# Performance work log

Hardware: AMD Instinct MI355X
Metric: run time of the kernel (lower is better)

## Reference

```python
import jax, jax.numpy as jnp
import numpy as np

B, S, H, NH = 8, 1024, 1024, 16
DH = H // NH


def setup_inputs() -> dict:
    key = jax.random.key(0)
    ks = jax.random.split(key, 16)
    inp = {
        'v': jax.random.normal(ks[0], (B, S, H), jnp.float32),
        'k': jax.random.normal(ks[1], (B, S, H), jnp.float32),
        'q': jax.random.normal(ks[2], (B, S, H), jnp.float32),
        'r': jax.random.normal(ks[3], (B, S, H), jnp.float32),
        'mask': jax.random.randint(ks[4], (B, 1, 1, S), 0, 2).astype(jnp.bool_),
    }
    scale = 1.0 / np.sqrt(H)
    names = ['Wv', 'Wk', 'Wq', 'Wr', 'Wm']
    for i, n in enumerate(names):
        inp[n] = jax.random.normal(ks[5 + i], (H, H), jnp.float32) * scale
        inp['b' + n[1:]] = jnp.zeros((H,), jnp.float32)
    return inp


def _heads(x, W, b):
    # torch Linear: x @ W.T + b, then split heads -> [B, NH, S, DH]
    y = jnp.einsum('bsh,oh->bso', x, W) + b
    return y.reshape(B, S, NH, DH).transpose(0, 2, 1, 3)


def reference(v, k, q, r, mask, Wv, bv, Wk, bk, Wq, bq, Wr, br, Wm, bm):
    vh = _heads(v, Wv, bv)
    kh = _heads(k, Wk, bk)
    qh = _heads(q, Wq, bq)
    rh = _heads(r, Wr, br)
    # relation-augmented scores: (QK^T + RK^T) / sqrt(d_k)
    scores = jnp.einsum('bhqd,bhkd->bhqk', qh + rh, kh) / jnp.sqrt(jnp.asarray(DH, qh.dtype))
    scores = jnp.where(mask, jnp.asarray(-1e9, scores.dtype), scores)
    att = jax.nn.softmax(scores, axis=-1)  # dropout = identity in eval
    out = jnp.einsum('bhqk,bhkd->bhqd', att, vh)
    out = out.transpose(0, 2, 1, 3).reshape(B, S, H)
    return jnp.einsum('bsh,oh->bso', out, Wm) + bm
```

## Files before the change

kernel.cpp:

```cpp
#include <hip/hip_runtime.h>
#include <hip/hip_bf16.h>
#include <stdint.h>

typedef __attribute__((ext_vector_type(4))) float f32x4;
typedef __attribute__((ext_vector_type(8))) short s16x8;
typedef __attribute__((ext_vector_type(4))) short s16x4;
typedef __attribute__((ext_vector_type(4))) int i32x4;

typedef const __attribute__((address_space(1))) unsigned glb_u32;
typedef __attribute__((address_space(3))) unsigned lds_u32;

#define DEVI __device__ __forceinline__

DEVI short f2b(float f) {
    union { float f; unsigned u; } v; v.f = f;
    unsigned r = v.u + 0x7fffu + ((v.u >> 16) & 1u);
    return (short)(r >> 16);
}

DEVI float vexp2(float x) {
    float r;
    asm("v_exp_f32 %0, %1" : "=v"(r) : "v"(x));
    return r;
}

DEVI unsigned cvtpk(float lo, float hi) {
    unsigned d;
    asm("v_cvt_pk_bf16_f32 %0, %1, %2" : "=v"(d) : "v"(lo), "v"(hi));
    return d;
}

DEVI s16x8 pack8(const f32x4& a, const f32x4& b) {
    union { unsigned u[4]; s16x8 v; } w;
    w.u[0] = cvtpk(a[0], a[1]);
    w.u[1] = cvtpk(a[2], a[3]);
    w.u[2] = cvtpk(b[0], b[1]);
    w.u[3] = cvtpk(b[2], b[3]);
    return w.v;
}

#define QSCL 0.18033688011112042f
#define MASKV -1.4426950408889634e9f

struct Ptr7 { const float* p[7]; };

__global__ __launch_bounds__(256) void cvt_all(Ptr7 t, short* __restrict__ vb,
                                               short* __restrict__ kb,
                                               short* __restrict__ Wb) {
    int bid = blockIdx.x;
    const float* s; short* d; int off;
    if (bid < 4096)      { s = t.p[0]; d = vb; off = bid; }
    else if (bid < 8192) { s = t.p[1]; d = kb; off = bid - 4096; }
    else {
        int w = (bid - 8192) >> 9;
        s = t.p[2 + w]; d = Wb + (size_t)w * 1048576u; off = (bid - 8192) & 511;
    }
    int i = (off * 256 + threadIdx.x) * 8;
    f32x4 a = *(const f32x4*)(s + i);
    f32x4 b = *(const f32x4*)(s + i + 4);
    *(s16x8*)(d + i) = pack8(a, b);
}

template<int AF32, int OUTMODE, int TWO>
DEVI void gemm_body(int logical,
                    const void* A0_, const void* A1_,
                    const short* W0, const short* W1,
                    const float* b0, const float* b1,
                    void* C_, short* As, short* Ws)
{
    constexpr int K = 1024, N = 1024;
    const int tid = threadIdx.x;
    const int lane = tid & 63, wid = tid >> 6;
    const int wm = wid >> 1, wn = wid & 1;
    const int r = lane & 15, g = lane >> 4;
    const int n0 = (logical & 7) * 128, m0 = (logical >> 3) * 128;

    auto stage_async = [&](int buf, int kt) {
        int kk = kt * 32;
        const short* Ap = (const short*)A0_; const short* Wp = W0;
        if (TWO && kk >= 1024) { Ap = (const short*)A1_; Wp = W1; kk &= 1023; }
#pragma unroll
        for (int i = 0; i < 2; ++i) {
            int row = wid * 32 + i * 16 + (lane >> 2);
            const short* ga = Ap + (size_t)(m0 + row) * K + kk + (lane & 3) * 8;
            const short* gw = Wp + (size_t)(n0 + row) * K + kk + (lane & 3) * 8;
            __builtin_amdgcn_global_load_lds((glb_u32*)ga,
                (lds_u32*)(As + buf * 4096 + (wid * 32 + i * 16) * 32), 16, 0, 0);
            __builtin_amdgcn_global_load_lds((glb_u32*)gw,
                (lds_u32*)(Ws + buf * 4096 + (wid * 32 + i * 16) * 32), 16, 0, 0);
        }
    };

    const int srow = tid >> 1, shalf = tid & 1;
    f32x4 a0g, a1g, a2g, a3g;
    s16x8 wg0, wg1;
    auto load_regs = [&](int kt) {
        int kk = kt * 32;
        const float* Ap = (const float*)A0_; const short* Wp = W0;
        if (TWO && kk >= 1024) { Ap = (const float*)A1_; Wp = W1; kk &= 1023; }
        const short* wp = Wp + (size_t)(n0 + srow) * K + kk + shalf * 16;
        wg0 = *(const s16x8*)wp;
        wg1 = *(const s16x8*)(wp + 8);
        const float* ap = Ap + (size_t)(m0 + srow) * K + kk + shalf * 16;
        a0g = *(const f32x4*)ap;       a1g = *(const f32x4*)(ap + 4);
        a2g = *(const f32x4*)(ap + 8); a3g = *(const f32x4*)(ap + 12);
    };
    auto store_lds = [&](int buf) {
        s16x8 s0 = pack8(a0g, a1g);
        s16x8 s1 = pack8(a2g, a3g);
        char* ab = (char*)(As + buf * 4096);
        *(s16x8*)(ab + srow * 64 + shalf * 32) = s0;
        *(s16x8*)(ab + srow * 64 + shalf * 32 + 16) = s1;
        char* wb = (char*)(Ws + buf * 4096);
        *(s16x8*)(wb + srow * 64 + shalf * 32) = wg0;
        *(s16x8*)(wb + srow * 64 + shalf * 32 + 16) = wg1;
    };

    f32x4 z = {0.f, 0.f, 0.f, 0.f};
    f32x4 acc[4][4];
#pragma unroll
    for (int i = 0; i < 4; ++i)
#pragma unroll
        for (int j = 0; j < 4; ++j) acc[i][j] = z;

    auto compute = [&](int buf) {
        s16x8 af[4], bfr[4];
#pragma unroll
        for (int f = 0; f < 4; ++f) {
            af[f]  = *(const s16x8*)(As + buf * 4096 + (wm * 64 + f * 16 + r) * 32 + g * 8);
            bfr[f] = *(const s16x8*)(Ws + buf * 4096 + (wn * 64 + f * 16 + r) * 32 + g * 8);
        }
#pragma unroll
        for (int i = 0; i < 4; ++i)
#pragma unroll
            for (int j = 0; j < 4; ++j)
                acc[i][j] = __builtin_amdgcn_mfma_f32_16x16x32_bf16(af[i], bfr[j], acc[i][j], 0, 0, 0);
    };

    constexpr int NK = TWO ? 64 : 32;
    if constexpr (AF32) { load_regs(0); store_lds(0); }
    else stage_async(0, 0);
    __syncthreads();
    int buf = 0;
    for (int kt = 0; kt < NK; ++kt) {
        if (kt + 1 < NK) {
            if constexpr (AF32) load_regs(kt + 1);
            else stage_async(buf ^ 1, kt + 1);
        }
        compute(buf);
        if (AF32 && kt + 1 < NK) store_lds(buf ^ 1);
        __syncthreads();
        buf ^= 1;
    }

#pragma unroll
    for (int j = 0; j < 4; ++j) {
        int col = n0 + wn * 64 + j * 16 + r;
        float bb = b0[col];
        if (TWO) bb += b1[col];
#pragma unroll
        for (int i = 0; i < 4; ++i) {
            int rowb = m0 + wm * 64 + i * 16 + g * 4;
            if constexpr (OUTMODE == 2) {
                int bb_ = rowb >> 10, tok = rowb & 1023;
                int tokp = (tok & ~31) | (((tok >> 2) & 3) << 3) | (((tok >> 4) & 1) << 2);
                short* dst = (short*)C_ + ((size_t)(bb_ * 16 + (col >> 6))) * 65536
                           + (size_t)(col & 63) * 1024 + tokp;
                s16x4 o;
#pragma unroll
                for (int q = 0; q < 4; ++q) o[q] = f2b(acc[i][j][q] + bb);
                *(s16x4*)dst = o;
            } else {
#pragma unroll
                for (int q = 0; q < 4; ++q) {
                    float val = acc[i][j][q] + bb;
                    if constexpr (OUTMODE == 1)
                        ((float*)C_)[(size_t)(rowb + q) * N + col] = val;
                    else if constexpr (OUTMODE == 3)
                        ((short*)C_)[(size_t)(rowb + q) * N + col] = f2b(val * QSCL);
                    else
                        ((short*)C_)[(size_t)(rowb + q) * N + col] = f2b(val);
                }
            }
        }
    }
}

__global__ __launch_bounds__(256) void proj_all(
    const short* __restrict__ vb, const short* __restrict__ kb,
    const float* __restrict__ qf, const float* __restrict__ rf,
    const short* __restrict__ Wb,
    const float* __restrict__ bv, const float* __restrict__ bk,
    const float* __restrict__ bq, const float* __restrict__ br,
    short* __restrict__ vtb, short* __restrict__ khb, short* __restrict__ qrb)
{
    __shared__ alignas(16) short As[2 * 128 * 32];
    __shared__ alignas(16) short Ws[2 * 128 * 32];
    const int bid = blockIdx.x;
    const int sub = bid >> 9, lbid = bid & 511;
    const int logical = (lbid & 7) * 64 + (lbid >> 3);
    if (sub == 0)
        gemm_body<0, 2, 0>(logical, vb, nullptr, Wb, nullptr, bv, nullptr, vtb, As, Ws);
    else if (sub == 1)
        gemm_body<0, 0, 0>(logical, kb, nullptr, Wb + 1048576u, nullptr, bk, nullptr, khb, As, Ws);
    else
        gemm_body<1, 3, 1>(logical, qf, rf, Wb + 2097152u, Wb + 3145728u, bq, br, qrb, As, Ws);
}

template<int AF32, int OUTMODE, int TWO>
__global__ __launch_bounds__(256) void gemm_nt(
    const void* __restrict__ A0_, const void* __restrict__ A1_,
    const short* __restrict__ W0, const short* __restrict__ W1,
    const float* __restrict__ b0, const float* __restrict__ b1,
    void* __restrict__ C_)
{
    __shared__ alignas(16) short As[2 * 128 * 32];
    __shared__ alignas(16) short Ws[2 * 128 * 32];
    const int bid = blockIdx.x;
    const int logical = (bid & 7) * 64 + (bid >> 3);
    gemm_body<AF32, OUTMODE, TWO>(logical, A0_, A1_, W0, W1, b0, b1, C_, As, Ws);
}

__global__ __launch_bounds__(256) void attn_fwd(
    const short* __restrict__ qrh, const short* __restrict__ kh,
    const short* __restrict__ vT, const int* __restrict__ mask,
    short* __restrict__ outp)
{
    const int bh = blockIdx.x;
    const int b = bh >> 4, h = bh & 15;
    const int qt = blockIdx.y;
    const int tid = threadIdx.x, lane = tid & 63, wid = tid >> 6;
    const int r = lane & 15, g = lane >> 4;

    __shared__ alignas(16) short Ks[64 * 64];
    __shared__ alignas(16) short Vs[64 * 64];
    __shared__ alignas(16) float mb[1024];

    {
        i32x4 mi = *(const i32x4*)(mask + b * 1024 + tid * 4);
        f32x4 mv;
#pragma unroll
        for (int j = 0; j < 4; ++j) mv[j] = mi[j] ? MASKV : 0.f;
        *(f32x4*)&mb[tid * 4] = mv;
    }

    const int q0 = qt * 128 + wid * 32;
    const short* qbA = qrh + (size_t)(b * 1024 + q0 + r) * 1024 + h * 64;
    const short* qbB = qbA + 16 * 1024;
    s16x8 qA0 = *(const s16x8*)(qbA + g * 8);
    s16x8 qA1 = *(const s16x8*)(qbA + 32 + g * 8);
    s16x8 qB0 = *(const s16x8*)(qbB + g * 8);
    s16x8 qB1 = *(const s16x8*)(qbB + 32 + g * 8);

    f32x4 z = {0.f, 0.f, 0.f, 0.f};
    f32x4 oA[4], oB[4];
#pragma unroll
    for (int i = 0; i < 4; ++i) { oA[i] = z; oB[i] = z; }
    float lA = 0.f, lB = 0.f;

    const int srow = tid >> 2, sq = tid & 3;
    const short* kg = kh + (size_t)(b * 1024 + srow) * 1024 + h * 64 + sq * 16;
    const short* vg = vT + ((size_t)(b * 16 + h)) * 65536 + (size_t)srow * 1024 + sq * 16;
    const int p0s = (sq * 2) ^ (srow & 7), p1s = (sq * 2 + 1) ^ (srow & 7);

    s16x8 kr0, kr1, vr0, vr1;
    auto stage_load = [&](int t) {
        const short* kp = kg + (size_t)(t * 64) * 1024;
        kr0 = *(const s16x8*)kp; kr1 = *(const s16x8*)(kp + 8);
        const short* vp = vg + t * 64;
        vr0 = *(const s16x8*)vp; vr1 = *(const s16x8*)(vp + 8);
    };
    auto stage_write = [&]() {
        char* kb2 = (char*)Ks;
        *(s16x8*)(kb2 + srow * 128 + p0s * 16) = kr0;
        *(s16x8*)(kb2 + srow * 128 + p1s * 16) = kr1;
        char* vb2 = (char*)Vs;
        *(s16x8*)(vb2 + srow * 128 + p0s * 16) = vr0;
        *(s16x8*)(vb2 + srow * 128 + p1s * 16) = vr1;
    };

    stage_load(0);
    for (int t = 0; t < 16; ++t) {
        if (t) __syncthreads();
        stage_write();
        __syncthreads();
        if (t < 15) stage_load(t + 1);

        f32x4 pA[4], pB[4];
        char* kb2 = (char*)Ks;
        float tsA = 0.f, tsB = 0.f;
#pragma unroll
        for (int fn = 0; fn < 4; ++fn) {
            int row = fn * 16 + r;
            s16x8 kfa = *(const s16x8*)(kb2 + row * 128 + ((g ^ (row & 7)) << 4));
            s16x8 kfb = *(const s16x8*)(kb2 + row * 128 + (((4 + g) ^ (row & 7)) << 4));
            f32x4 cA = __builtin_amdgcn_mfma_f32_16x16x32_bf16(kfa, qA0, z, 0, 0, 0);
            cA = __builtin_amdgcn_mfma_f32_16x16x32_bf16(kfb, qA1, cA, 0, 0, 0);
            f32x4 cB = __builtin_amdgcn_mfma_f32_16x16x32_bf16(kfa, qB0, z, 0, 0, 0);
            cB = __builtin_amdgcn_mfma_f32_16x16x32_bf16(kfb, qB1, cB, 0, 0, 0);
            f32x4 mv = *(const f32x4*)&mb[t * 64 + fn * 16 + g * 4];
#pragma unroll
            for (int qi = 0; qi < 4; ++qi) {
                float eA = vexp2(cA[qi] + mv[qi]); pA[fn][qi] = eA; tsA += eA;
                float eB = vexp2(cB[qi] + mv[qi]); pB[fn][qi] = eB; tsB += eB;
            }
        }
        tsA += __shfl_xor(tsA, 16); tsA += __shfl_xor(tsA, 32);
        tsB += __shfl_xor(tsB, 16); tsB += __shfl_xor(tsB, 32);
        lA += tsA; lB += tsB;

        char* vb2 = (char*)Vs;
#pragma unroll
        for (int ks = 0; ks < 2; ++ks) {
            s16x8 pbA = pack8(pA[2 * ks], pA[2 * ks + 1]);
            s16x8 pbB = pack8(pB[2 * ks], pB[2 * ks + 1]);
#pragma unroll
            for (int df = 0; df < 4; ++df) {
                int row = df * 16 + r;
                int slot = (ks * 4 + g) ^ (row & 7);
                s16x8 vf = *(const s16x8*)(vb2 + row * 128 + (slot << 4));
                oA[df] = __builtin_amdgcn_mfma_f32_16x16x32_bf16(vf, pbA, oA[df], 0, 0, 0);
                oB[df] = __builtin_amdgcn_mfma_f32_16x16x32_bf16(vf, pbB, oB[df], 0, 0, 0);
            }
        }
    }

    float ivA = 1.f / lA, ivB = 1.f / lB;
#pragma unroll
    for (int df = 0; df < 4; ++df) {
        s16x4 oa, ob;
#pragma unroll
        for (int qi = 0; qi < 4; ++qi) {
            oa[qi] = f2b(oA[df][qi] * ivA);
            ob[qi] = f2b(oB[df][qi] * ivB);
        }
        *(s16x4*)&outp[(size_t)(b * 1024 + q0 + r) * 1024 + h * 64 + df * 16 + g * 4] = oa;
        *(s16x4*)&outp[(size_t)(b * 1024 + q0 + 16 + r) * 1024 + h * 64 + df * 16 + g * 4] = ob;
    }
}

extern "C" void kernel_launch(void* const* d_in, const int* in_sizes, int n_in,
                              void* d_out, int out_size, void* d_ws, size_t ws_size,
                              hipStream_t stream) {
    const float* v  = (const float*)d_in[0];
    const float* k  = (const float*)d_in[1];
    const float* q  = (const float*)d_in[2];
    const float* rr = (const float*)d_in[3];
    const int* mask = (const int*)d_in[4];
    const float* Wv = (const float*)d_in[5];  const float* bv = (const float*)d_in[6];
    const float* Wk = (const float*)d_in[7];  const float* bk = (const float*)d_in[8];
    const float* Wq = (const float*)d_in[9];  const float* bq = (const float*)d_in[10];
    const float* Wr = (const float*)d_in[11]; const float* br = (const float*)d_in[12];
    const float* Wm = (const float*)d_in[13]; const float* bm = (const float*)d_in[14];

    const size_t MB = 1048576u;
    const size_t NEED = 90u * MB;
    if (ws_size < NEED) return;

    char* ws = (char*)d_ws;
    short* Wb  = (short*)ws;
    short* vb  = (short*)(ws + 10u * MB);
    short* kb  = (short*)(ws + 26u * MB);
    short* vtb = (short*)(ws + 42u * MB);
    short* khb = (short*)(ws + 58u * MB);
    short* qrb = (short*)(ws + 74u * MB);
    short* att = vb;

    Ptr7 t7;
    t7.p[0] = v;  t7.p[1] = k;
    t7.p[2] = Wv; t7.p[3] = Wk; t7.p[4] = Wq; t7.p[5] = Wr; t7.p[6] = Wm;
    cvt_all<<<dim3(10752), 256, 0, stream>>>(t7, vb, kb, Wb);

    proj_all<<<dim3(1536), 256, 0, stream>>>(vb, kb, q, rr, Wb,
                                             bv, bk, bq, br, vtb, khb, qrb);

    attn_fwd<<<dim3(128, 8), 256, 0, stream>>>(qrb, khb, vtb, mask, att);

    gemm_nt<0, 1, 0><<<dim3(512), 256, 0, stream>>>(att, nullptr, Wb + 4194304u,
                                                    nullptr, bm, nullptr, (float*)d_out);
}
```

Baseline: 223.3 us.

## Use 256-row M tiles for V and K projections in fused projection kernel

The V and K projection GEMMs inside proj_all now use 256x128 output tiles, with each wave computing 128x64 (8x4 MFMA fragments). This halves their block count, so the combined launch drops from 1536 to 1024 blocks while the Q+R GEMM keeps 128x128 tiles. The aim is more reuse of each weight tile per load and less global traffic. In exchange the kernel uses more LDS and accumulator registers, which lowers occupancy for every block, including the Q+R path that shares the kernel.

```diff
diff --git a/kernel.cpp b/kernel.cpp
--- a/kernel.cpp
+++ b/kernel.cpp
@@ -61,7 +61,7 @@
     *(s16x8*)(d + i) = pack8(a, b);
 }
 
-template<int AF32, int OUTMODE, int TWO>
+template<int AF32, int OUTMODE, int TWO, int FAT>
 DEVI void gemm_body(int logical,
                     const void* A0_, const void* A1_,
                     const short* W0, const short* W1,
@@ -69,25 +69,33 @@
                     void* C_, short* As, short* Ws)
 {
     constexpr int K = 1024, N = 1024;
+    constexpr int BM   = FAT ? 256 : 128;
+    constexpr int MI   = FAT ? 8 : 4;
+    constexpr int WMS  = FAT ? 128 : 64;
+    constexpr int ABUF = BM * 32;
     const int tid = threadIdx.x;
     const int lane = tid & 63, wid = tid >> 6;
     const int wm = wid >> 1, wn = wid & 1;
     const int r = lane & 15, g = lane >> 4;
-    const int n0 = (logical & 7) * 128, m0 = (logical >> 3) * 128;
+    const int n0 = (logical & 7) * 128, m0 = (logical >> 3) * BM;
 
     auto stage_async = [&](int buf, int kt) {
         int kk = kt * 32;
         const short* Ap = (const short*)A0_; const short* Wp = W0;
         if (TWO && kk >= 1024) { Ap = (const short*)A1_; Wp = W1; kk &= 1023; }
 #pragma unroll
+        for (int i = 0; i < (FAT ? 4 : 2); ++i) {
+            int rbase = wid * (FAT ? 64 : 32) + i * 16;
+            const short* ga = Ap + (size_t)(m0 + rbase + (lane >> 2)) * K + kk + (lane & 3) * 8;
+            __builtin_amdgcn_global_load_lds((glb_u32*)ga,
+                (lds_u32*)(As + buf * ABUF + rbase * 32), 16, 0, 0);
+        }
+#pragma unroll
         for (int i = 0; i < 2; ++i) {
-            int row = wid * 32 + i * 16 + (lane >> 2);
-            const short* ga = Ap + (size_t)(m0 + row) * K + kk + (lane & 3) * 8;
-            const short* gw = Wp + (size_t)(n0 + row) * K + kk + (lane & 3) * 8;
-            __builtin_amdgcn_global_load_lds((glb_u32*)ga,
-                (lds_u32*)(As + buf * 4096 + (wid * 32 + i * 16) * 32), 16, 0, 0);
+            int rbase = wid * 32 + i * 16;
+            const short* gw = Wp + (size_t)(n0 + rbase + (lane >> 2)) * K + kk + (lane & 3) * 8;
             __builtin_amdgcn_global_load_lds((glb_u32*)gw,
-                (lds_u32*)(Ws + buf * 4096 + (wid * 32 + i * 16) * 32), 16, 0, 0);
+                (lds_u32*)(Ws + buf * 4096 + rbase * 32), 16, 0, 0);
         }
     };
 
@@ -108,7 +116,7 @@
     auto store_lds = [&](int buf) {
         s16x8 s0 = pack8(a0g, a1g);
         s16x8 s1 = pack8(a2g, a3g);
-        char* ab = (char*)(As + buf * 4096);
+        char* ab = (char*)(As + buf * ABUF);
         *(s16x8*)(ab + srow * 64 + shalf * 32) = s0;
         *(s16x8*)(ab + srow * 64 + shalf * 32 + 16) = s1;
         char* wb = (char*)(Ws + buf * 4096);
@@ -117,21 +125,22 @@
     };
 
     f32x4 z = {0.f, 0.f, 0.f, 0.f};
-    f32x4 acc[4][4];
-#pragma unroll
-    for (int i = 0; i < 4; ++i)
+    f32x4 acc[MI][4];
+#pragma unroll
+    for (int i = 0; i < MI; ++i)
 #pragma unroll
         for (int j = 0; j < 4; ++j) acc[i][j] = z;
 
     auto compute = [&](int buf) {
-        s16x8 af[4], bfr[4];
-#pragma unroll
-        for (int f = 0; f < 4; ++f) {
-            af[f]  = *(const s16x8*)(As + buf * 4096 + (wm * 64 + f * 16 + r) * 32 + g * 8);
+        s16x8 af[MI], bfr[4];
+#pragma unroll
+        for (int f = 0; f < MI; ++f)
+            af[f] = *(const s16x8*)(As + buf * ABUF + (wm * WMS + f * 16 + r) * 32 + g * 8);
+#pragma unroll
+        for (int f = 0; f < 4; ++f)
             bfr[f] = *(const s16x8*)(Ws + buf * 4096 + (wn * 64 + f * 16 + r) * 32 + g * 8);
-        }
-#pragma unroll
-        for (int i = 0; i < 4; ++i)
+#pragma unroll
+        for (int i = 0; i < MI; ++i)
 #pragma unroll
             for (int j = 0; j < 4; ++j)
                 acc[i][j] = __builtin_amdgcn_mfma_f32_16x16x32_bf16(af[i], bfr[j], acc[i][j], 0, 0, 0);
@@ -159,8 +168,8 @@
         float bb = b0[col];
         if (TWO) bb += b1[col];
 #pragma unroll
-        for (int i = 0; i < 4; ++i) {
-            int rowb = m0 + wm * 64 + i * 16 + g * 4;
+        for (int i = 0; i < MI; ++i) {
+            int rowb = m0 + wm * WMS + i * 16 + g * 4;
             if constexpr (OUTMODE == 2) {
                 int bb_ = rowb >> 10, tok = rowb & 1023;
                 int tokp = (tok & ~31) | (((tok >> 2) & 3) << 3) | (((tok >> 4) & 1) << 2);
@@ -194,17 +203,22 @@
     const float* __restrict__ bq, const float* __restrict__ br,
     short* __restrict__ vtb, short* __restrict__ khb, short* __restrict__ qrb)
 {
-    __shared__ alignas(16) short As[2 * 128 * 32];
+    __shared__ alignas(16) short As[2 * 256 * 32];
     __shared__ alignas(16) short Ws[2 * 128 * 32];
     const int bid = blockIdx.x;
-    const int sub = bid >> 9, lbid = bid & 511;
-    const int logical = (lbid & 7) * 64 + (lbid >> 3);
-    if (sub == 0)
-        gemm_body<0, 2, 0>(logical, vb, nullptr, Wb, nullptr, bv, nullptr, vtb, As, Ws);
-    else if (sub == 1)
-        gemm_body<0, 0, 0>(logical, kb, nullptr, Wb + 1048576u, nullptr, bk, nullptr, khb, As, Ws);
-    else
-        gemm_body<1, 3, 1>(logical, qf, rf, Wb + 2097152u, Wb + 3145728u, bq, br, qrb, As, Ws);
+    if (bid < 256) {
+        int lb = bid;
+        int logical = (lb & 7) * 32 + (lb >> 3);
+        gemm_body<0, 2, 0, 1>(logical, vb, nullptr, Wb, nullptr, bv, nullptr, vtb, As, Ws);
+    } else if (bid < 512) {
+        int lb = bid - 256;
+        int logical = (lb & 7) * 32 + (lb >> 3);
+        gemm_body<0, 0, 0, 1>(logical, kb, nullptr, Wb + 1048576u, nullptr, bk, nullptr, khb, As, Ws);
+    } else {
+        int lb = bid - 512;
+        int logical = (lb & 7) * 64 + (lb >> 3);
+        gemm_body<1, 3, 1, 0>(logical, qf, rf, Wb + 2097152u, Wb + 3145728u, bq, br, qrb, As, Ws);
+    }
 }
 
 template<int AF32, int OUTMODE, int TWO>
@@ -218,7 +232,7 @@
     __shared__ alignas(16) short Ws[2 * 128 * 32];
     const int bid = blockIdx.x;
     const int logical = (bid & 7) * 64 + (bid >> 3);
-    gemm_body<AF32, OUTMODE, TWO>(logical, A0_, A1_, W0, W1, b0, b1, C_, As, Ws);
+    gemm_body<AF32, OUTMODE, TWO, 0>(logical, A0_, A1_, W0, W1, b0, b1, C_, As, Ws);
 }
 
 __global__ __launch_bounds__(256) void attn_fwd(
@@ -371,7 +385,7 @@
     t7.p[2] = Wv; t7.p[3] = Wk; t7.p[4] = Wq; t7.p[5] = Wr; t7.p[6] = Wm;
     cvt_all<<<dim3(10752), 256, 0, stream>>>(t7, vb, kb, Wb);
 
-    proj_all<<<dim3(1536), 256, 0, stream>>>(vb, kb, q, rr, Wb,
+    proj_all<<<dim3(1024), 256, 0, stream>>>(vb, kb, q, rr, Wb,
                                              bv, bk, bq, br, vtb, khb, qrb);
 
     attn_fwd<<<dim3(128, 8), 256, 0, stream>>>(qrb, khb, vtb, mask, att);
```

Measured after the change: 232.9 us. 4.3% more time.

## Replace LDS-staged GEMM with direct-from-global register-prefetch GEMM and pre-convert q/r

Applied to the files above, without the earlier changes.

The GEMM body no longer stages tiles through shared memory. Each wave loads its MFMA fragments straight from global memory into registers, double-buffered across k-steps, so the __syncthreads barriers go away. The fp32 q and r inputs are now converted to bf16 in the conversion kernel, and the projection is split into separate q/r and v/k launches, with outputs aliased into the freed buffers. The trade-off is that each wave re-reads operands from global memory with no LDS reuse across waves in a block, which leans on L2 and raises global traffic. The extra conversion pass also adds bytes written and read.

```diff
diff --git a/kernel.cpp b/kernel.cpp
--- a/kernel.cpp
+++ b/kernel.cpp
@@ -6,9 +6,6 @@
 typedef __attribute__((ext_vector_type(8))) short s16x8;
 typedef __attribute__((ext_vector_type(4))) short s16x4;
 typedef __attribute__((ext_vector_type(4))) int i32x4;
-
-typedef const __attribute__((address_space(1))) unsigned glb_u32;
-typedef __attribute__((address_space(3))) unsigned lds_u32;
 
 #define DEVI __device__ __forceinline__
 
@@ -42,18 +39,22 @@
 #define QSCL 0.18033688011112042f
 #define MASKV -1.4426950408889634e9f
 
-struct Ptr7 { const float* p[7]; };
-
-__global__ __launch_bounds__(256) void cvt_all(Ptr7 t, short* __restrict__ vb,
+struct Ptr9 { const float* p[9]; };
+
+__global__ __launch_bounds__(256) void cvt_all(Ptr9 t, short* __restrict__ vb,
                                                short* __restrict__ kb,
+                                               short* __restrict__ qb,
+                                               short* __restrict__ rb,
                                                short* __restrict__ Wb) {
     int bid = blockIdx.x;
     const float* s; short* d; int off;
-    if (bid < 4096)      { s = t.p[0]; d = vb; off = bid; }
-    else if (bid < 8192) { s = t.p[1]; d = kb; off = bid - 4096; }
+    if (bid < 4096)       { s = t.p[0]; d = vb; off = bid; }
+    else if (bid < 8192)  { s = t.p[1]; d = kb; off = bid - 4096; }
+    else if (bid < 12288) { s = t.p[2]; d = qb; off = bid - 8192; }
+    else if (bid < 16384) { s = t.p[3]; d = rb; off = bid - 12288; }
     else {
-        int w = (bid - 8192) >> 9;
-        s = t.p[2 + w]; d = Wb + (size_t)w * 1048576u; off = (bid - 8192) & 511;
+        int w = (bid - 16384) >> 9;
+        s = t.p[4 + w]; d = Wb + (size_t)w * 1048576u; off = (bid - 16384) & 511;
     }
     int i = (off * 256 + threadIdx.x) * 8;
     f32x4 a = *(const f32x4*)(s + i);
@@ -61,12 +62,11 @@
     *(s16x8*)(d + i) = pack8(a, b);
 }
 
-template<int AF32, int OUTMODE, int TWO>
-DEVI void gemm_body(int logical,
-                    const void* A0_, const void* A1_,
-                    const short* W0, const short* W1,
-                    const float* b0, const float* b1,
-                    void* C_, short* As, short* Ws)
+template<int OUTMODE, int TWO>
+DEVI void dgemm_body(int logical,
+                     const short* A0, const short* A1,
+                     const short* W0, const short* W1,
+                     const float* b0, const float* b1, void* C_)
 {
     constexpr int K = 1024, N = 1024;
     const int tid = threadIdx.x;
@@ -75,47 +75,6 @@
     const int r = lane & 15, g = lane >> 4;
     const int n0 = (logical & 7) * 128, m0 = (logical >> 3) * 128;
 
-    auto stage_async = [&](int buf, int kt) {
-        int kk = kt * 32;
-        const short* Ap = (const short*)A0_; const short* Wp = W0;
-        if (TWO && kk >= 1024) { Ap = (const short*)A1_; Wp = W1; kk &= 1023; }
-#pragma unroll
-        for (int i = 0; i < 2; ++i) {
-            int row = wid * 32 + i * 16 + (lane >> 2);
-            const short* ga = Ap + (size_t)(m0 + row) * K + kk + (lane & 3) * 8;
-            const short* gw = Wp + (size_t)(n0 + row) * K + kk + (lane & 3) * 8;
-            __builtin_amdgcn_global_load_lds((glb_u32*)ga,
-                (lds_u32*)(As + buf * 4096 + (wid * 32 + i * 16) * 32), 16, 0, 0);
-            __builtin_amdgcn_global_load_lds((glb_u32*)gw,
-                (lds_u32*)(Ws + buf * 4096 + (wid * 32 + i * 16) * 32), 16, 0, 0);
-        }
-    };
-
-    const int srow = tid >> 1, shalf = tid & 1;
-    f32x4 a0g, a1g, a2g, a3g;
-    s16x8 wg0, wg1;
-    auto load_regs = [&](int kt) {
-        int kk = kt * 32;
-        const float* Ap = (const float*)A0_; const short* Wp = W0;
-        if (TWO && kk >= 1024) { Ap = (const float*)A1_; Wp = W1; kk &= 1023; }
-        const short* wp = Wp + (size_t)(n0 + srow) * K + kk + shalf * 16;
-        wg0 = *(const s16x8*)wp;
-        wg1 = *(const s16x8*)(wp + 8);
-        const float* ap = Ap + (size_t)(m0 + srow) * K + kk + shalf * 16;
-        a0g = *(const f32x4*)ap;       a1g = *(const f32x4*)(ap + 4);
-        a2g = *(const f32x4*)(ap + 8); a3g = *(const f32x4*)(ap + 12);
-    };
-    auto store_lds = [&](int buf) {
-        s16x8 s0 = pack8(a0g, a1g);
-        s16x8 s1 = pack8(a2g, a3g);
-        char* ab = (char*)(As + buf * 4096);
-        *(s16x8*)(ab + srow * 64 + shalf * 32) = s0;
-        *(s16x8*)(ab + srow * 64 + shalf * 32 + 16) = s1;
-        char* wb = (char*)(Ws + buf * 4096);
-        *(s16x8*)(wb + srow * 64 + shalf * 32) = wg0;
-        *(s16x8*)(wb + srow * 64 + shalf * 32 + 16) = wg1;
-    };
-
     f32x4 z = {0.f, 0.f, 0.f, 0.f};
     f32x4 acc[4][4];
 #pragma unroll
@@ -123,35 +82,48 @@
 #pragma unroll
         for (int j = 0; j < 4; ++j) acc[i][j] = z;
 
-    auto compute = [&](int buf) {
-        s16x8 af[4], bfr[4];
+    auto half = [&](const short* Ap, const short* Wp) {
+        const short* ab[4];
+        const short* wb[4];
 #pragma unroll
         for (int f = 0; f < 4; ++f) {
-            af[f]  = *(const s16x8*)(As + buf * 4096 + (wm * 64 + f * 16 + r) * 32 + g * 8);
-            bfr[f] = *(const s16x8*)(Ws + buf * 4096 + (wn * 64 + f * 16 + r) * 32 + g * 8);
-        }
-#pragma unroll
-        for (int i = 0; i < 4; ++i)
-#pragma unroll
-            for (int j = 0; j < 4; ++j)
-                acc[i][j] = __builtin_amdgcn_mfma_f32_16x16x32_bf16(af[i], bfr[j], acc[i][j], 0, 0, 0);
+            ab[f] = Ap + (size_t)(m0 + wm * 64 + f * 16 + r) * K + g * 8;
+            wb[f] = Wp + (size_t)(n0 + wn * 64 + f * 16 + r) * K + g * 8;
+        }
+        s16x8 aX[4], wX[4], aY[4], wY[4];
+#pragma unroll
+        for (int f = 0; f < 4; ++f) {
+            aX[f] = *(const s16x8*)ab[f];
+            wX[f] = *(const s16x8*)wb[f];
+        }
+#pragma unroll
+        for (int kt = 0; kt < 32; kt += 2) {
+#pragma unroll
+            for (int f = 0; f < 4; ++f) {
+                aY[f] = *(const s16x8*)(ab[f] + (kt + 1) * 32);
+                wY[f] = *(const s16x8*)(wb[f] + (kt + 1) * 32);
+            }
+#pragma unroll
+            for (int i = 0; i < 4; ++i)
+#pragma unroll
+                for (int j = 0; j < 4; ++j)
+                    acc[i][j] = __builtin_amdgcn_mfma_f32_16x16x32_bf16(aX[i], wX[j], acc[i][j], 0, 0, 0);
+            if (kt + 2 < 32) {
+#pragma unroll
+                for (int f = 0; f < 4; ++f) {
+                    aX[f] = *(const s16x8*)(ab[f] + (kt + 2) * 32);
+                    wX[f] = *(const s16x8*)(wb[f] + (kt + 2) * 32);
+                }
+            }
+#pragma unroll
+            for (int i = 0; i < 4; ++i)
+#pragma unroll
+                for (int j = 0; j < 4; ++j)
+                    acc[i][j] = __builtin_amdgcn_mfma_f32_16x16x32_bf16(aY[i], wY[j], acc[i][j], 0, 0, 0);
+        }
     };
-
-    constexpr int NK = TWO ? 64 : 32;
-    if constexpr (AF32) { load_regs(0); store_lds(0); }
-    else stage_async(0, 0);
-    __syncthreads();
-    int buf = 0;
-    for (int kt = 0; kt < NK; ++kt) {
-        if (kt + 1 < NK) {
-            if constexpr (AF32) load_regs(kt + 1);
-            else stage_async(buf ^ 1, kt + 1);
-        }
-        compute(buf);
-        if (AF32 && kt + 1 < NK) store_lds(buf ^ 1);
-        __syncthreads();
-        buf ^= 1;
-    }
+    half(A0, W0);
+    if constexpr (TWO) half(A1, W1);
 
 #pragma unroll
     for (int j = 0; j < 4; ++j) {
@@ -186,39 +158,39 @@
     }
 }
 
-__global__ __launch_bounds__(256) void proj_all(
+__global__ __launch_bounds__(256) void proj_qr(
+    const short* __restrict__ qb, const short* __restrict__ rb,
+    const short* __restrict__ Wq, const short* __restrict__ Wr,
+    const float* __restrict__ bq, const float* __restrict__ br,
+    short* __restrict__ qrb)
+{
+    const int bid = blockIdx.x;
+    const int logical = (bid & 7) * 64 + (bid >> 3);
+    dgemm_body<3, 1>(logical, qb, rb, Wq, Wr, bq, br, qrb);
+}
+
+__global__ __launch_bounds__(256) void proj_vk(
     const short* __restrict__ vb, const short* __restrict__ kb,
-    const float* __restrict__ qf, const float* __restrict__ rf,
     const short* __restrict__ Wb,
     const float* __restrict__ bv, const float* __restrict__ bk,
-    const float* __restrict__ bq, const float* __restrict__ br,
-    short* __restrict__ vtb, short* __restrict__ khb, short* __restrict__ qrb)
-{
-    __shared__ alignas(16) short As[2 * 128 * 32];
-    __shared__ alignas(16) short Ws[2 * 128 * 32];
+    short* __restrict__ vtb, short* __restrict__ khb)
+{
     const int bid = blockIdx.x;
-    const int sub = bid >> 9, lbid = bid & 511;
-    const int logical = (lbid & 7) * 64 + (lbid >> 3);
-    if (sub == 0)
-        gemm_body<0, 2, 0>(logical, vb, nullptr, Wb, nullptr, bv, nullptr, vtb, As, Ws);
-    else if (sub == 1)
-        gemm_body<0, 0, 0>(logical, kb, nullptr, Wb + 1048576u, nullptr, bk, nullptr, khb, As, Ws);
+    const int lb = bid & 511;
+    const int logical = (lb & 7) * 64 + (lb >> 3);
+    if (bid < 512)
+        dgemm_body<2, 0>(logical, vb, nullptr, Wb, nullptr, bv, nullptr, vtb);
     else
-        gemm_body<1, 3, 1>(logical, qf, rf, Wb + 2097152u, Wb + 3145728u, bq, br, qrb, As, Ws);
-}
-
-template<int AF32, int OUTMODE, int TWO>
-__global__ __launch_bounds__(256) void gemm_nt(
-    const void* __restrict__ A0_, const void* __restrict__ A1_,
-    const short* __restrict__ W0, const short* __restrict__ W1,
-    const float* __restrict__ b0, const float* __restrict__ b1,
-    void* __restrict__ C_)
-{
-    __shared__ alignas(16) short As[2 * 128 * 32];
-    __shared__ alignas(16) short Ws[2 * 128 * 32];
+        dgemm_body<0, 0>(logical, kb, nullptr, Wb + 1048576u, nullptr, bk, nullptr, khb);
+}
+
+__global__ __launch_bounds__(256) void gemm_out(
+    const short* __restrict__ att, const short* __restrict__ Wm,
+    const float* __restrict__ bm, float* __restrict__ out)
+{
     const int bid = blockIdx.x;
     const int logical = (bid & 7) * 64 + (bid >> 3);
-    gemm_body<AF32, OUTMODE, TWO>(logical, A0_, A1_, W0, W1, b0, b1, C_, As, Ws);
+    dgemm_body<1, 0>(logical, att, nullptr, Wm, nullptr, bm, nullptr, out);
 }
 
 __global__ __launch_bounds__(256) void attn_fwd(
@@ -361,21 +333,23 @@
     short* Wb  = (short*)ws;
     short* vb  = (short*)(ws + 10u * MB);
     short* kb  = (short*)(ws + 26u * MB);
-    short* vtb = (short*)(ws + 42u * MB);
-    short* khb = (short*)(ws + 58u * MB);
+    short* qb  = (short*)(ws + 42u * MB);
+    short* rb  = (short*)(ws + 58u * MB);
     short* qrb = (short*)(ws + 74u * MB);
+    short* vtb = qb;
+    short* khb = rb;
     short* att = vb;
 
-    Ptr7 t7;
-    t7.p[0] = v;  t7.p[1] = k;
-    t7.p[2] = Wv; t7.p[3] = Wk; t7.p[4] = Wq; t7.p[5] = Wr; t7.p[6] = Wm;
-    cvt_all<<<dim3(10752), 256, 0, stream>>>(t7, vb, kb, Wb);
-
-    proj_all<<<dim3(1536), 256, 0, stream>>>(vb, kb, q, rr, Wb,
-                                             bv, bk, bq, br, vtb, khb, qrb);
+    Ptr9 t9;
+    t9.p[0] = v;  t9.p[1] = k;  t9.p[2] = q;  t9.p[3] = rr;
+    t9.p[4] = Wv; t9.p[5] = Wk; t9.p[6] = Wq; t9.p[7] = Wr; t9.p[8] = Wm;
+    cvt_all<<<dim3(18944), 256, 0, stream>>>(t9, vb, kb, qb, rb, Wb);
+
+    proj_qr<<<dim3(512), 256, 0, stream>>>(qb, rb, Wb + 2097152u, Wb + 3145728u,
+                                           bq, br, qrb);
+    proj_vk<<<dim3(1024), 256, 0, stream>>>(vb, kb, Wb, bv, bk, vtb, khb);
 
     attn_fwd<<<dim3(128, 8), 256, 0, stream>>>(qrb, khb, vtb, mask, att);
 
-    gemm_nt<0, 1, 0><<<dim3(512), 256, 0, stream>>>(att, nullptr, Wb + 4194304u,
-                                                    nullptr, bm, nullptr, (float*)d_out);
-}
+    gemm_out<<<dim3(512), 256, 0, stream>>>(att, Wb + 4194304u, bm, (float*)d_out);
+}
```

After: 380.8 us. 70.6% more time.

## Swizzle GEMM LDS layout and triple-buffer async loads with vmcnt waits

Applied to the files above, without the earlier changes.

Applies an XOR swizzle to the 16-byte chunks in the A/W LDS tiles, on the async global_load_lds path, the register store path and the MFMA fragment reads, to cut LDS bank conflicts. The bf16-input GEMM path moves from double buffering with a full __syncthreads per step to a three-stage ring: it prefetches two tiles ahead, waits with s_waitcnt vmcnt(4) and uses a bare s_barrier. This raises LDS use per block (48KB), which may reduce occupancy. The output GEMM becomes a non-template wrapper kernel.

```diff
diff --git a/kernel.cpp b/kernel.cpp
--- a/kernel.cpp
+++ b/kernel.cpp
@@ -75,19 +75,21 @@
     const int r = lane & 15, g = lane >> 4;
     const int n0 = (logical & 7) * 128, m0 = (logical >> 3) * 128;
 
-    auto stage_async = [&](int buf, int kt) {
+    const int arow = lane >> 2;
+    const int lq8 = ((lane & 3) ^ ((lane >> 3) & 3)) * 8;
+    auto stage = [&](int buf, int kt) {
         int kk = kt * 32;
         const short* Ap = (const short*)A0_; const short* Wp = W0;
         if (TWO && kk >= 1024) { Ap = (const short*)A1_; Wp = W1; kk &= 1023; }
 #pragma unroll
         for (int i = 0; i < 2; ++i) {
-            int row = wid * 32 + i * 16 + (lane >> 2);
-            const short* ga = Ap + (size_t)(m0 + row) * K + kk + (lane & 3) * 8;
-            const short* gw = Wp + (size_t)(n0 + row) * K + kk + (lane & 3) * 8;
+            int rbase = wid * 32 + i * 16;
+            const short* ga = Ap + (size_t)(m0 + rbase + arow) * K + kk + lq8;
+            const short* gw = Wp + (size_t)(n0 + rbase + arow) * K + kk + lq8;
             __builtin_amdgcn_global_load_lds((glb_u32*)ga,
-                (lds_u32*)(As + buf * 4096 + (wid * 32 + i * 16) * 32), 16, 0, 0);
+                (lds_u32*)(As + buf * 4096 + rbase * 32), 16, 0, 0);
             __builtin_amdgcn_global_load_lds((glb_u32*)gw,
-                (lds_u32*)(Ws + buf * 4096 + (wid * 32 + i * 16) * 32), 16, 0, 0);
+                (lds_u32*)(Ws + buf * 4096 + rbase * 32), 16, 0, 0);
         }
     };
 
@@ -108,12 +110,14 @@
     auto store_lds = [&](int buf) {
         s16x8 s0 = pack8(a0g, a1g);
         s16x8 s1 = pack8(a2g, a3g);
+        int sw = (srow >> 1) & 3;
+        int ph0 = (shalf * 2) ^ sw, ph1 = (shalf * 2 + 1) ^ sw;
         char* ab = (char*)(As + buf * 4096);
-        *(s16x8*)(ab + srow * 64 + shalf * 32) = s0;
-        *(s16x8*)(ab + srow * 64 + shalf * 32 + 16) = s1;
+        *(s16x8*)(ab + srow * 64 + ph0 * 16) = s0;
+        *(s16x8*)(ab + srow * 64 + ph1 * 16) = s1;
         char* wb = (char*)(Ws + buf * 4096);
-        *(s16x8*)(wb + srow * 64 + shalf * 32) = wg0;
-        *(s16x8*)(wb + srow * 64 + shalf * 32 + 16) = wg1;
+        *(s16x8*)(wb + srow * 64 + ph0 * 16) = wg0;
+        *(s16x8*)(wb + srow * 64 + ph1 * 16) = wg1;
     };
 
     f32x4 z = {0.f, 0.f, 0.f, 0.f};
@@ -123,12 +127,13 @@
 #pragma unroll
         for (int j = 0; j < 4; ++j) acc[i][j] = z;
 
+    const int sl = (g ^ ((r >> 1) & 3)) << 3;
     auto compute = [&](int buf) {
         s16x8 af[4], bfr[4];
 #pragma unroll
         for (int f = 0; f < 4; ++f) {
-            af[f]  = *(const s16x8*)(As + buf * 4096 + (wm * 64 + f * 16 + r) * 32 + g * 8);
-            bfr[f] = *(const s16x8*)(Ws + buf * 4096 + (wn * 64 + f * 16 + r) * 32 + g * 8);
+            af[f]  = *(const s16x8*)(As + buf * 4096 + (wm * 64 + f * 16 + r) * 32 + sl);
+            bfr[f] = *(const s16x8*)(Ws + buf * 4096 + (wn * 64 + f * 16 + r) * 32 + sl);
         }
 #pragma unroll
         for (int i = 0; i < 4; ++i)
@@ -138,19 +143,27 @@
     };
 
     constexpr int NK = TWO ? 64 : 32;
-    if constexpr (AF32) { load_regs(0); store_lds(0); }
-    else stage_async(0, 0);
-    __syncthreads();
-    int buf = 0;
-    for (int kt = 0; kt < NK; ++kt) {
-        if (kt + 1 < NK) {
-            if constexpr (AF32) load_regs(kt + 1);
-            else stage_async(buf ^ 1, kt + 1);
-        }
-        compute(buf);
-        if (AF32 && kt + 1 < NK) store_lds(buf ^ 1);
+    if constexpr (AF32) {
+        load_regs(0); store_lds(0);
         __syncthreads();
-        buf ^= 1;
+        int buf = 0;
+        for (int kt = 0; kt < NK; ++kt) {
+            if (kt + 1 < NK) load_regs(kt + 1);
+            compute(buf);
+            if (kt + 1 < NK) store_lds(buf ^ 1);
+            __syncthreads();
+            buf ^= 1;
+        }
+    } else {
+        stage(0, 0);
+        stage(1, 1);
+        for (int t = 0; t < NK; ++t) {
+            if (t + 1 < NK) asm volatile("s_waitcnt vmcnt(4)" ::: "memory");
+            else            asm volatile("s_waitcnt vmcnt(0)" ::: "memory");
+            __builtin_amdgcn_s_barrier();
+            if (t + 2 < NK) stage((t + 2) % 3, t + 2);
+            compute(t % 3);
+        }
     }
 
 #pragma unroll
@@ -194,11 +207,11 @@
     const float* __restrict__ bq, const float* __restrict__ br,
     short* __restrict__ vtb, short* __restrict__ khb, short* __restrict__ qrb)
 {
-    __shared__ alignas(16) short As[2 * 128 * 32];
-    __shared__ alignas(16) short Ws[2 * 128 * 32];
+    __shared__ alignas(16) short As[3 * 4096];
+    __shared__ alignas(16) short Ws[3 * 4096];
     const int bid = blockIdx.x;
-    const int sub = bid >> 9, lbid = bid & 511;
-    const int logical = (lbid & 7) * 64 + (lbid >> 3);
+    const int sub = bid >> 9, lb = bid & 511;
+    const int logical = (lb & 7) * 64 + (lb >> 3);
     if (sub == 0)
         gemm_body<0, 2, 0>(logical, vb, nullptr, Wb, nullptr, bv, nullptr, vtb, As, Ws);
     else if (sub == 1)
@@ -207,18 +220,15 @@
         gemm_body<1, 3, 1>(logical, qf, rf, Wb + 2097152u, Wb + 3145728u, bq, br, qrb, As, Ws);
 }
 
-template<int AF32, int OUTMODE, int TWO>
-__global__ __launch_bounds__(256) void gemm_nt(
-    const void* __restrict__ A0_, const void* __restrict__ A1_,
-    const short* __restrict__ W0, const short* __restrict__ W1,
-    const float* __restrict__ b0, const float* __restrict__ b1,
-    void* __restrict__ C_)
+__global__ __launch_bounds__(256) void gemm_out(
+    const short* __restrict__ att, const short* __restrict__ Wm,
+    const float* __restrict__ bm, float* __restrict__ out)
 {
-    __shared__ alignas(16) short As[2 * 128 * 32];
-    __shared__ alignas(16) short Ws[2 * 128 * 32];
+    __shared__ alignas(16) short As[3 * 4096];
+    __shared__ alignas(16) short Ws[3 * 4096];
     const int bid = blockIdx.x;
     const int logical = (bid & 7) * 64 + (bid >> 3);
-    gemm_body<AF32, OUTMODE, TWO>(logical, A0_, A1_, W0, W1, b0, b1, C_, As, Ws);
+    gemm_body<0, 1, 0>(logical, att, nullptr, Wm, nullptr, bm, nullptr, out, As, Ws);
 }
 
 __global__ __launch_bounds__(256) void attn_fwd(
@@ -376,6 +386,5 @@
 
     attn_fwd<<<dim3(128, 8), 256, 0, stream>>>(qrb, khb, vtb, mask, att);
 
-    gemm_nt<0, 1, 0><<<dim3(512), 256, 0, stream>>>(att, nullptr, Wb + 4194304u,
-                                                    nullptr, bm, nullptr, (float*)d_out);
-}
+    gemm_out<<<dim3(512), 256, 0, stream>>>(att, Wb + 4194304u, bm, (float*)d_out);
+}
```

New measurement: 230.0 us. 1.03x slower.
